# Kernel tuning notes

Measured on AMD Instinct MI355X. Metric: run time of the kernel, lower is better.

Reference implementation:

```python
import jax, jax.numpy as jnp
import numpy as np

NUM_ENTITIES = 100000
NUM_RELATIONS = 8
HIDDEN = 128
N_NODES = 100000
N_EDGES = 500000


def setup_inputs() -> dict:
    key = jax.random.key(0)
    ks = jax.random.split(key, 10)
    scale = 1.0 / np.sqrt(HIDDEN)
    inp = {
        "x_ids": jax.random.randint(ks[0], (N_NODES,), 0, NUM_ENTITIES),
        "edge_index": jax.random.randint(ks[1], (2, N_EDGES), 0, N_NODES),
        "edge_type": jax.random.randint(ks[2], (N_EDGES,), 0, NUM_RELATIONS),
        "emb": jax.random.normal(ks[3], (NUM_ENTITIES, HIDDEN), jnp.float32),
        "W1": jax.random.normal(ks[4], (NUM_RELATIONS, HIDDEN, HIDDEN), jnp.float32) * scale,
        "root1": jax.random.normal(ks[5], (HIDDEN, HIDDEN), jnp.float32) * scale,
        "b1": jnp.zeros((HIDDEN,), jnp.float32),
        "W2": jax.random.normal(ks[6], (NUM_RELATIONS, HIDDEN, HIDDEN), jnp.float32) * scale,
        "root2": jax.random.normal(ks[7], (HIDDEN, HIDDEN), jnp.float32) * scale,
        "b2": jnp.zeros((HIDDEN,), jnp.float32),
    }
    return inp


def rgcn_conv(x, edge_index, edge_type, W, root, bias):
    # x: [N, d]; W: [R, d, d]; PyG RGCNConv with aggr='mean' (per-relation mean)
    N, d = x.shape
    R = W.shape[0]
    src, dst = edge_index[0], edge_index[1]
    # transform every node under every relation: [N, R, d]
    h = jnp.einsum('nd,rdf->nrf', x, W)
    msg = h[src, edge_type]                       # [E, d] gather per edge
    seg = dst * R + edge_type                     # composite (node, relation) segment id
    sums = jax.ops.segment_sum(msg, seg, num_segments=N * R)
    cnt = jax.ops.segment_sum(jnp.ones((msg.shape[0], 1), x.dtype), seg, num_segments=N * R)
    agg = (sums / jnp.maximum(cnt, 1.0)).reshape(N, R, d).sum(axis=1)
    return agg + x @ root + bias


def reference(x_ids, edge_index, edge_type, emb, W1, root1, b1, W2, root2, b2):
    x = emb[x_ids]                                # embedding lookup [N, d]
    x = rgcn_conv(x, edge_index, edge_type, W1, root1, b1)
    x = jax.nn.relu(x)
    x = rgcn_conv(x, edge_index, edge_type, W2, root2, b2)
    return jax.nn.sigmoid(x)
```

## Files before the change

### kernel.cpp

```cpp
#include <hip/hip_runtime.h>

#define HD 128
#define RNUM 8
#define SCAN_BS 2048

typedef __attribute__((ext_vector_type(8))) short short8;
typedef __attribute__((ext_vector_type(4))) float float4e;

__device__ __forceinline__ unsigned short f2bf(float f) {
    unsigned int u = __float_as_uint(f);
    u += 0x7fffu + ((u >> 16) & 1u);
    return (unsigned short)(u >> 16);
}

__device__ __forceinline__ void acc2(float4e& a, unsigned int u, int i) {
    a[i]     += __uint_as_float(u << 16);
    a[i + 1] += __uint_as_float(u & 0xffff0000u);
}

__device__ __forceinline__ void gload_lds16(const void* g, void* l) {
    __builtin_amdgcn_global_load_lds(
        (const __attribute__((address_space(1))) void*)g,
        (__attribute__((address_space(3))) void*)l, 16, 0, 0);
}

__global__ void zero_i(int* __restrict__ p, int n) {
    int g = blockIdx.x * blockDim.x + threadIdx.x;
    if (g < n) p[g] = 0;
}

__global__ void tobf16_kernel(const float* __restrict__ in, unsigned short* __restrict__ out,
                              long long n8) {
    long long g = (long long)blockIdx.x * blockDim.x + threadIdx.x;
    if (g >= n8) return;
    const float4* p = (const float4*)(in + g * 8);
    float4 v0 = p[0], v1 = p[1];
    uint4 o;
    o.x = (unsigned int)f2bf(v0.x) | ((unsigned int)f2bf(v0.y) << 16);
    o.y = (unsigned int)f2bf(v0.z) | ((unsigned int)f2bf(v0.w) << 16);
    o.z = (unsigned int)f2bf(v1.x) | ((unsigned int)f2bf(v1.y) << 16);
    o.w = (unsigned int)f2bf(v1.z) | ((unsigned int)f2bf(v1.w) << 16);
    *(uint4*)(out + g * 8) = o;
}

__global__ void count_kernel(const int* __restrict__ ei, const int* __restrict__ et,
                             int* __restrict__ cnt, int E, int N) {
    int e = blockIdx.x * blockDim.x + threadIdx.x;
    if (e < E) atomicAdd(&cnt[et[e] * N + ei[E + e]], 1);
}

__global__ void scan1(const int* __restrict__ in, int* __restrict__ out,
                      int* __restrict__ bsum, int n) {
    __shared__ int s[256];
    const int tid = threadIdx.x;
    const int base = blockIdx.x * SCAN_BS + tid * 8;
    int v[8];
    int sum = 0;
#pragma unroll
    for (int j = 0; j < 8; j++) {
        int x = (base + j < n) ? in[base + j] : 0;
        v[j] = sum;
        sum += x;
    }
    s[tid] = sum;
    __syncthreads();
    for (int off = 1; off < 256; off <<= 1) {
        int tv = (tid >= off) ? s[tid - off] : 0;
        __syncthreads();
        if (tid >= off) s[tid] += tv;
        __syncthreads();
    }
    int excl = (tid > 0) ? s[tid - 1] : 0;
    if (tid == 255) bsum[blockIdx.x] = s[255];
#pragma unroll
    for (int j = 0; j < 8; j++)
        if (base + j < n) out[base + j] = v[j] + excl;
}

__global__ void scan2(int* __restrict__ bsum, int nb) {
    __shared__ int s[512];
    const int tid = threadIdx.x;
    s[tid] = (tid < nb) ? bsum[tid] : 0;
    __syncthreads();
    for (int off = 1; off < 512; off <<= 1) {
        int tv = (tid >= off) ? s[tid - off] : 0;
        __syncthreads();
        if (tid >= off) s[tid] += tv;
        __syncthreads();
    }
    if (tid < nb) bsum[tid] = (tid > 0) ? s[tid - 1] : 0;
}

__global__ void scan3(int* __restrict__ out, int* __restrict__ cur,
                      const int* __restrict__ bsum, int n) {
    const int base = blockIdx.x * SCAN_BS + threadIdx.x * 8;
    const int add = bsum[blockIdx.x];
#pragma unroll
    for (int j = 0; j < 8; j++) {
        int i = base + j;
        if (i < n) {
            int v = out[i] + add;
            out[i] = v;
            cur[i] = v;
        }
    }
}

__global__ void fill_kernel(const int* __restrict__ ei, const int* __restrict__ et,
                            const int* __restrict__ ids,
                            int* __restrict__ cur, int* __restrict__ col,
                            int* __restrict__ colE, int E, int N) {
    int e = blockIdx.x * blockDim.x + threadIdx.x;
    if (e < E) {
        int src = ei[e];
        int pos = atomicAdd(&cur[et[e] * N + ei[E + e]], 1);
        col[pos] = src;
        colE[pos] = ids[src];
    }
}

__global__ void wt_all(const float* __restrict__ W1, const float* __restrict__ r1,
                       const float* __restrict__ W2, const float* __restrict__ r2,
                       unsigned short* __restrict__ WT) {
    int g = blockIdx.x * blockDim.x + threadIdx.x;
    if (g >= 18 * 16384) return;
    int mat = g >> 14;
    int idx = g & 16383;
    int d = idx >> 7;
    int f = idx & 127;
    const float* src;
    int m;
    if (mat < 8)       { src = W1; m = mat; }
    else if (mat == 8) { src = r1; m = 0; }
    else if (mat < 17) { src = W2; m = mat - 9; }
    else               { src = r2; m = 0; }
    WT[mat * 16384 + f * 128 + d] = f2bf(src[(size_t)m * 16384 + d * 128 + f]);
}

template <bool HAS_IDX, int ACT>
__launch_bounds__(256, 3)
__global__ void rgcn_fused(const int* __restrict__ row_start, const int* __restrict__ col,
                           const int* __restrict__ ids,
                           const unsigned short* __restrict__ x16,
                           const unsigned short* __restrict__ WT,
                           const float* __restrict__ bias,
                           void* __restrict__ CoutV, int N, int E) {
    __shared__ unsigned short As[64 * 128];
    __shared__ unsigned short Ws[128 * 128];

    const int tid = threadIdx.x;
    const int block0 = blockIdx.x * 64;
    const int w = tid >> 6;
    const int lane = tid & 63;
    const int ln15 = lane & 15;
    const int quad = lane >> 4;
    const int rowbase = (w & 1) * 32;
    const int colbase = (w >> 1) * 64;
    const int grp = tid >> 3;
    const int sub8 = tid & 7;

    float4e acc[2][4];
#pragma unroll
    for (int i = 0; i < 2; i++)
#pragma unroll
        for (int j = 0; j < 4; j++)
#pragma unroll
            for (int q = 0; q < 4; q++) acc[i][j][q] = 0.0f;

    for (int s = 0; s < 9; s++) {
        {
            const unsigned short* Wsrc = WT + s * 16384;
#pragma unroll
            for (int i = 0; i < 8; i++) {
                int c = i * 256 + tid;
                int f = c >> 4;
                int cc = c & 15;
                const void* src = (const void*)(Wsrc + f * 128 + ((cc ^ (f & 15)) << 3));
                int cbase = i * 256 + (tid & ~63);
                gload_lds16(src, (char*)Ws + (size_t)cbase * 16);
            }
        }
        if (s < RNUM) {
#pragma unroll 1
            for (int half = 0; half < 2; half++) {
                const int row = grp + half * 32;
                const int dst = block0 + row;
                float4e a0 = {0.f, 0.f, 0.f, 0.f};
                float4e a1 = {0.f, 0.f, 0.f, 0.f};
                float4e a2 = {0.f, 0.f, 0.f, 0.f};
                float4e a3 = {0.f, 0.f, 0.f, 0.f};
                float inv = 0.f;
                if (dst < N) {
                    int seg = s * N + dst;
                    int s0 = row_start[seg];
                    int s1 = (seg == RNUM * N - 1) ? E : row_start[seg + 1];
                    if (s1 > s0) inv = 1.0f / (float)(s1 - s0);
                    for (int e = s0; e < s1; e++) {
                        int c = col[e];
                        const uint4* xp = (const uint4*)(x16 + (size_t)c * HD + sub8 * 16);
                        uint4 v0 = xp[0];
                        uint4 v1 = xp[1];
                        acc2(a0, v0.x, 0); acc2(a0, v0.y, 2);
                        acc2(a1, v0.z, 0); acc2(a1, v0.w, 2);
                        acc2(a2, v1.x, 0); acc2(a2, v1.y, 2);
                        acc2(a3, v1.z, 0); acc2(a3, v1.w, 2);
                    }
                }
                a0 *= inv; a1 *= inv; a2 *= inv; a3 *= inv;
                uint4 o0, o1;
                o0.x = (unsigned int)f2bf(a0[0]) | ((unsigned int)f2bf(a0[1]) << 16);
                o0.y = (unsigned int)f2bf(a0[2]) | ((unsigned int)f2bf(a0[3]) << 16);
                o0.z = (unsigned int)f2bf(a1[0]) | ((unsigned int)f2bf(a1[1]) << 16);
                o0.w = (unsigned int)f2bf(a1[2]) | ((unsigned int)f2bf(a1[3]) << 16);
                o1.x = (unsigned int)f2bf(a2[0]) | ((unsigned int)f2bf(a2[1]) << 16);
                o1.y = (unsigned int)f2bf(a2[2]) | ((unsigned int)f2bf(a2[3]) << 16);
                o1.z = (unsigned int)f2bf(a3[0]) | ((unsigned int)f2bf(a3[1]) << 16);
                o1.w = (unsigned int)f2bf(a3[2]) | ((unsigned int)f2bf(a3[3]) << 16);
                const int ck0 = sub8 * 2;
                *(uint4*)&As[row * 128 + ((ck0 ^ (row & 15)) << 3)] = o0;
                *(uint4*)&As[row * 128 + (((ck0 + 1) ^ (row & 15)) << 3)] = o1;
            }
        } else {
#pragma unroll 1
            for (int half = 0; half < 2; half++) {
                const int row = grp + half * 32;
                const int dst = block0 + row;
                uint4 o0 = {0u, 0u, 0u, 0u}, o1 = {0u, 0u, 0u, 0u};
                if (dst < N) {
                    int srcn = HAS_IDX ? ids[dst] : dst;
                    const uint4* xp = (const uint4*)(x16 + (size_t)srcn * HD + sub8 * 16);
                    o0 = xp[0];
                    o1 = xp[1];
                }
                const int ck0 = sub8 * 2;
                *(uint4*)&As[row * 128 + ((ck0 ^ (row & 15)) << 3)] = o0;
                *(uint4*)&As[row * 128 + (((ck0 + 1) ^ (row & 15)) << 3)] = o1;
            }
        }
        __syncthreads();

#pragma unroll
        for (int k0 = 0; k0 < 4; k0++) {
            short8 af[2], bf[4];
            const int ck = k0 * 4 + quad;
#pragma unroll
            for (int rt = 0; rt < 2; rt++) {
                int m = rowbase + rt * 16 + ln15;
                af[rt] = *(const short8*)&As[m * 128 + ((ck ^ (m & 15)) << 3)];
            }
#pragma unroll
            for (int ct = 0; ct < 4; ct++) {
                int n = colbase + ct * 16 + ln15;
                bf[ct] = *(const short8*)&Ws[n * 128 + ((ck ^ (n & 15)) << 3)];
            }
#pragma unroll
            for (int rt = 0; rt < 2; rt++)
#pragma unroll
                for (int ct = 0; ct < 4; ct++)
                    acc[rt][ct] = __builtin_amdgcn_mfma_f32_16x16x32_bf16(
                        af[rt], bf[ct], acc[rt][ct], 0, 0, 0);
        }
        __syncthreads();
    }

#pragma unroll
    for (int ct = 0; ct < 4; ct++) {
        int ncol = colbase + ct * 16 + ln15;
        float bv = bias[ncol];
#pragma unroll
        for (int rt = 0; rt < 2; rt++) {
#pragma unroll
            for (int rg = 0; rg < 4; rg++) {
                int rowg = block0 + rowbase + rt * 16 + quad * 4 + rg;
                if (rowg < N) {
                    float v = acc[rt][ct][rg] + bv;
                    if (ACT == 0) {
                        v = fmaxf(v, 0.0f);
                        ((unsigned short*)CoutV)[(size_t)rowg * HD + ncol] = f2bf(v);
                    } else {
                        v = 1.0f / (1.0f + expf(-v));
                        ((float*)CoutV)[(size_t)rowg * HD + ncol] = v;
                    }
                }
            }
        }
    }
}

extern "C" void kernel_launch(void* const* d_in, const int* in_sizes, int n_in,
                              void* d_out, int out_size, void* d_ws, size_t ws_size,
                              hipStream_t stream) {
    const int*   x_ids = (const int*)d_in[0];
    const int*   ei    = (const int*)d_in[1];
    const int*   et    = (const int*)d_in[2];
    const float* emb   = (const float*)d_in[3];
    const float* W1    = (const float*)d_in[4];
    const float* root1 = (const float*)d_in[5];
    const float* b1    = (const float*)d_in[6];
    const float* W2    = (const float*)d_in[7];
    const float* root2 = (const float*)d_in[8];
    const float* b2    = (const float*)d_in[9];

    const int N = in_sizes[0];
    const int E = in_sizes[1] / 2;
    const int NS = RNUM * N;
    const long long embElems = (long long)in_sizes[3];
    float* out = (float*)d_out;

    char* ws = (char*)d_ws;
    size_t off = 0;
    int* row_start = (int*)(ws + off); off += (size_t)NS * 4;
    int* col       = (int*)(ws + off); off += (size_t)E * 4;
    int* colE      = (int*)(ws + off); off += (size_t)E * 4;
    int* bsum      = (int*)(ws + off); off += 4096;
    unsigned short* WT    = (unsigned short*)(ws + off); off += (size_t)18 * 16384 * 2;
    unsigned short* emb16 = (unsigned short*)(ws + off); off += (size_t)embElems * 2;
    unsigned short* z16   = (unsigned short*)(ws + off); off += (size_t)N * HD * 2;
    int* cur = (int*)z16;

    const int scanBlocks = (NS + SCAN_BS - 1) / SCAN_BS;
    const int layerGrid = (N + 63) / 64;

    zero_i<<<(NS + 255) / 256, 256, 0, stream>>>(cur, NS);
    count_kernel<<<(E + 255) / 256, 256, 0, stream>>>(ei, et, cur, E, N);
    scan1<<<scanBlocks, 256, 0, stream>>>(cur, row_start, bsum, NS);
    scan2<<<1, 512, 0, stream>>>(bsum, scanBlocks);
    scan3<<<scanBlocks, 256, 0, stream>>>(row_start, cur, bsum, NS);
    fill_kernel<<<(E + 255) / 256, 256, 0, stream>>>(ei, et, x_ids, cur, col, colE, E, N);

    wt_all<<<(18 * 16384 + 255) / 256, 256, 0, stream>>>(W1, root1, W2, root2, WT);

    {
        long long n8 = embElems / 8;
        tobf16_kernel<<<(unsigned int)((n8 + 255) / 256), 256, 0, stream>>>(emb, emb16, n8);
    }

    rgcn_fused<true, 0><<<layerGrid, 256, 0, stream>>>(
        row_start, colE, x_ids, emb16, WT, b1, (void*)z16, N, E);
    rgcn_fused<false, 1><<<layerGrid, 256, 0, stream>>>(
        row_start, col, nullptr, z16, WT + 9 * 16384, b2, (void*)out, N, E);
}
```

Measured before the change: 459.9 us.

## Use node-major CSR segments, 4-thread row gather, and merge prep kernels

Segment ids become dst*8+rel instead of rel*N+dst, so each node's eight relation ranges sit next to each other in row_start and the end offset is read directly from a sentinel entry. The fused layer kernel now assigns four threads per destination row, each loading 64 bytes of a neighbour's features, which replaces the two-pass half loop. The root-weight stage is moved out of the relation loop. The weight transpose and embedding bf16 conversion are merged into one launch to save a kernel launch. Fewer threads per row means fewer gathers in flight per row and more register pressure from eight accumulators.

Result: faster. 407.8 us (-11.3%).

```diff
diff --git a/kernel.cpp b/kernel.cpp
--- a/kernel.cpp
+++ b/kernel.cpp
@@ -13,6 +13,10 @@
     return (unsigned short)(u >> 16);
 }
 
+__device__ __forceinline__ unsigned int pk2(float lo, float hi) {
+    return (unsigned int)f2bf(lo) | ((unsigned int)f2bf(hi) << 16);
+}
+
 __device__ __forceinline__ void acc2(float4e& a, unsigned int u, int i) {
     a[i]     += __uint_as_float(u << 16);
     a[i + 1] += __uint_as_float(u & 0xffff0000u);
@@ -29,24 +33,43 @@
     if (g < n) p[g] = 0;
 }
 
-__global__ void tobf16_kernel(const float* __restrict__ in, unsigned short* __restrict__ out,
-                              long long n8) {
+__global__ void prep_kernel(const float* __restrict__ W1, const float* __restrict__ r1,
+                            const float* __restrict__ W2, const float* __restrict__ r2,
+                            unsigned short* __restrict__ WT,
+                            const float* __restrict__ emb, unsigned short* __restrict__ emb16,
+                            long long n8) {
     long long g = (long long)blockIdx.x * blockDim.x + threadIdx.x;
-    if (g >= n8) return;
-    const float4* p = (const float4*)(in + g * 8);
-    float4 v0 = p[0], v1 = p[1];
-    uint4 o;
-    o.x = (unsigned int)f2bf(v0.x) | ((unsigned int)f2bf(v0.y) << 16);
-    o.y = (unsigned int)f2bf(v0.z) | ((unsigned int)f2bf(v0.w) << 16);
-    o.z = (unsigned int)f2bf(v1.x) | ((unsigned int)f2bf(v1.y) << 16);
-    o.w = (unsigned int)f2bf(v1.z) | ((unsigned int)f2bf(v1.w) << 16);
-    *(uint4*)(out + g * 8) = o;
+    if (g < 18 * 16384) {
+        int gi = (int)g;
+        int mat = gi >> 14;
+        int idx = gi & 16383;
+        int d = idx >> 7;
+        int f = idx & 127;
+        const float* src;
+        int m;
+        if (mat < 8)       { src = W1; m = mat; }
+        else if (mat == 8) { src = r1; m = 0; }
+        else if (mat < 17) { src = W2; m = mat - 9; }
+        else               { src = r2; m = 0; }
+        WT[mat * 16384 + f * 128 + d] = f2bf(src[(size_t)m * 16384 + d * 128 + f]);
+    }
+    long long h = g - 18 * 16384;
+    if (h >= 0 && h < n8) {
+        const float4* p = (const float4*)(emb + h * 8);
+        float4 v0 = p[0], v1 = p[1];
+        uint4 o;
+        o.x = pk2(v0.x, v0.y);
+        o.y = pk2(v0.z, v0.w);
+        o.z = pk2(v1.x, v1.y);
+        o.w = pk2(v1.z, v1.w);
+        *(uint4*)(emb16 + h * 8) = o;
+    }
 }
 
 __global__ void count_kernel(const int* __restrict__ ei, const int* __restrict__ et,
                              int* __restrict__ cnt, int E, int N) {
     int e = blockIdx.x * blockDim.x + threadIdx.x;
-    if (e < E) atomicAdd(&cnt[et[e] * N + ei[E + e]], 1);
+    if (e < E) atomicAdd(&cnt[ei[E + e] * RNUM + et[e]], 1);
 }
 
 __global__ void scan1(const int* __restrict__ in, int* __restrict__ out,
@@ -109,32 +132,16 @@
 __global__ void fill_kernel(const int* __restrict__ ei, const int* __restrict__ et,
                             const int* __restrict__ ids,
                             int* __restrict__ cur, int* __restrict__ col,
-                            int* __restrict__ colE, int E, int N) {
+                            int* __restrict__ colE, int* __restrict__ row_start,
+                            int E, int N) {
     int e = blockIdx.x * blockDim.x + threadIdx.x;
+    if (e == 0) row_start[RNUM * N] = E;
     if (e < E) {
         int src = ei[e];
-        int pos = atomicAdd(&cur[et[e] * N + ei[E + e]], 1);
+        int pos = atomicAdd(&cur[ei[E + e] * RNUM + et[e]], 1);
         col[pos] = src;
         colE[pos] = ids[src];
     }
-}
-
-__global__ void wt_all(const float* __restrict__ W1, const float* __restrict__ r1,
-                       const float* __restrict__ W2, const float* __restrict__ r2,
-                       unsigned short* __restrict__ WT) {
-    int g = blockIdx.x * blockDim.x + threadIdx.x;
-    if (g >= 18 * 16384) return;
-    int mat = g >> 14;
-    int idx = g & 16383;
-    int d = idx >> 7;
-    int f = idx & 127;
-    const float* src;
-    int m;
-    if (mat < 8)       { src = W1; m = mat; }
-    else if (mat == 8) { src = r1; m = 0; }
-    else if (mat < 17) { src = W2; m = mat - 9; }
-    else               { src = r2; m = 0; }
-    WT[mat * 16384 + f * 128 + d] = f2bf(src[(size_t)m * 16384 + d * 128 + f]);
 }
 
 template <bool HAS_IDX, int ACT>
@@ -156,8 +163,10 @@
     const int quad = lane >> 4;
     const int rowbase = (w & 1) * 32;
     const int colbase = (w >> 1) * 64;
-    const int grp = tid >> 3;
-    const int sub8 = tid & 7;
+    const int grp = tid >> 2;
+    const int sub4 = tid & 3;
+    const int mydst = block0 + grp;
+    const bool rowok = (mydst < N);
 
     float4e acc[2][4];
 #pragma unroll
@@ -167,7 +176,8 @@
 #pragma unroll
             for (int q = 0; q < 4; q++) acc[i][j][q] = 0.0f;
 
-    for (int s = 0; s < 9; s++) {
+#pragma unroll 1
+    for (int s = 0; s < RNUM; s++) {
         {
             const unsigned short* Wsrc = WT + s * 16384;
 #pragma unroll
@@ -180,65 +190,91 @@
                 gload_lds16(src, (char*)Ws + (size_t)cbase * 16);
             }
         }
-        if (s < RNUM) {
-#pragma unroll 1
-            for (int half = 0; half < 2; half++) {
-                const int row = grp + half * 32;
-                const int dst = block0 + row;
-                float4e a0 = {0.f, 0.f, 0.f, 0.f};
-                float4e a1 = {0.f, 0.f, 0.f, 0.f};
-                float4e a2 = {0.f, 0.f, 0.f, 0.f};
-                float4e a3 = {0.f, 0.f, 0.f, 0.f};
-                float inv = 0.f;
-                if (dst < N) {
-                    int seg = s * N + dst;
-                    int s0 = row_start[seg];
-                    int s1 = (seg == RNUM * N - 1) ? E : row_start[seg + 1];
-                    if (s1 > s0) inv = 1.0f / (float)(s1 - s0);
-                    for (int e = s0; e < s1; e++) {
-                        int c = col[e];
-                        const uint4* xp = (const uint4*)(x16 + (size_t)c * HD + sub8 * 16);
-                        uint4 v0 = xp[0];
-                        uint4 v1 = xp[1];
-                        acc2(a0, v0.x, 0); acc2(a0, v0.y, 2);
-                        acc2(a1, v0.z, 0); acc2(a1, v0.w, 2);
-                        acc2(a2, v1.x, 0); acc2(a2, v1.y, 2);
-                        acc2(a3, v1.z, 0); acc2(a3, v1.w, 2);
-                    }
-                }
-                a0 *= inv; a1 *= inv; a2 *= inv; a3 *= inv;
-                uint4 o0, o1;
-                o0.x = (unsigned int)f2bf(a0[0]) | ((unsigned int)f2bf(a0[1]) << 16);
-                o0.y = (unsigned int)f2bf(a0[2]) | ((unsigned int)f2bf(a0[3]) << 16);
-                o0.z = (unsigned int)f2bf(a1[0]) | ((unsigned int)f2bf(a1[1]) << 16);
-                o0.w = (unsigned int)f2bf(a1[2]) | ((unsigned int)f2bf(a1[3]) << 16);
-                o1.x = (unsigned int)f2bf(a2[0]) | ((unsigned int)f2bf(a2[1]) << 16);
-                o1.y = (unsigned int)f2bf(a2[2]) | ((unsigned int)f2bf(a2[3]) << 16);
-                o1.z = (unsigned int)f2bf(a3[0]) | ((unsigned int)f2bf(a3[1]) << 16);
-                o1.w = (unsigned int)f2bf(a3[2]) | ((unsigned int)f2bf(a3[3]) << 16);
-                const int ck0 = sub8 * 2;
-                *(uint4*)&As[row * 128 + ((ck0 ^ (row & 15)) << 3)] = o0;
-                *(uint4*)&As[row * 128 + (((ck0 + 1) ^ (row & 15)) << 3)] = o1;
-            }
-        } else {
-#pragma unroll 1
-            for (int half = 0; half < 2; half++) {
-                const int row = grp + half * 32;
-                const int dst = block0 + row;
-                uint4 o0 = {0u, 0u, 0u, 0u}, o1 = {0u, 0u, 0u, 0u};
-                if (dst < N) {
-                    int srcn = HAS_IDX ? ids[dst] : dst;
-                    const uint4* xp = (const uint4*)(x16 + (size_t)srcn * HD + sub8 * 16);
-                    o0 = xp[0];
-                    o1 = xp[1];
-                }
-                const int ck0 = sub8 * 2;
-                *(uint4*)&As[row * 128 + ((ck0 ^ (row & 15)) << 3)] = o0;
-                *(uint4*)&As[row * 128 + (((ck0 + 1) ^ (row & 15)) << 3)] = o1;
-            }
-        }
-        __syncthreads();
-
+        {
+            float4e a[8];
+#pragma unroll
+            for (int j = 0; j < 8; j++) a[j] = (float4e){0.f, 0.f, 0.f, 0.f};
+            int s0 = 0, s1 = 0;
+            if (rowok) {
+                s0 = row_start[mydst * 8 + s];
+                s1 = row_start[mydst * 8 + s + 1];
+            }
+            const float inv = (s1 > s0) ? 1.0f / (float)(s1 - s0) : 0.0f;
+            for (int e = s0; e < s1; e++) {
+                int c = col[e];
+                const uint4* xp = (const uint4*)(x16 + (size_t)c * HD + sub4 * 32);
+                uint4 v0 = xp[0], v1 = xp[1], v2 = xp[2], v3 = xp[3];
+                acc2(a[0], v0.x, 0); acc2(a[0], v0.y, 2);
+                acc2(a[1], v0.z, 0); acc2(a[1], v0.w, 2);
+                acc2(a[2], v1.x, 0); acc2(a[2], v1.y, 2);
+                acc2(a[3], v1.z, 0); acc2(a[3], v1.w, 2);
+                acc2(a[4], v2.x, 0); acc2(a[4], v2.y, 2);
+                acc2(a[5], v2.z, 0); acc2(a[5], v2.w, 2);
+                acc2(a[6], v3.x, 0); acc2(a[6], v3.y, 2);
+                acc2(a[7], v3.z, 0); acc2(a[7], v3.w, 2);
+            }
+#pragma unroll
+            for (int j = 0; j < 8; j++) a[j] *= inv;
+#pragma unroll
+            for (int j = 0; j < 4; j++) {
+                uint4 o;
+                o.x = pk2(a[2 * j][0], a[2 * j][1]);
+                o.y = pk2(a[2 * j][2], a[2 * j][3]);
+                o.z = pk2(a[2 * j + 1][0], a[2 * j + 1][1]);
+                o.w = pk2(a[2 * j + 1][2], a[2 * j + 1][3]);
+                int ck = sub4 * 4 + j;
+                *(uint4*)&As[grp * 128 + ((ck ^ (grp & 15)) << 3)] = o;
+            }
+        }
+        __syncthreads();
+
+#pragma unroll
+        for (int k0 = 0; k0 < 4; k0++) {
+            short8 af[2], bf[4];
+            const int ck = k0 * 4 + quad;
+#pragma unroll
+            for (int rt = 0; rt < 2; rt++) {
+                int m = rowbase + rt * 16 + ln15;
+                af[rt] = *(const short8*)&As[m * 128 + ((ck ^ (m & 15)) << 3)];
+            }
+#pragma unroll
+            for (int ct = 0; ct < 4; ct++) {
+                int n = colbase + ct * 16 + ln15;
+                bf[ct] = *(const short8*)&Ws[n * 128 + ((ck ^ (n & 15)) << 3)];
+            }
+#pragma unroll
+            for (int rt = 0; rt < 2; rt++)
+#pragma unroll
+                for (int ct = 0; ct < 4; ct++)
+                    acc[rt][ct] = __builtin_amdgcn_mfma_f32_16x16x32_bf16(
+                        af[rt], bf[ct], acc[rt][ct], 0, 0, 0);
+        }
+        __syncthreads();
+    }
+
+    {
+        const unsigned short* Wsrc = WT + RNUM * 16384;
+#pragma unroll
+        for (int i = 0; i < 8; i++) {
+            int c = i * 256 + tid;
+            int f = c >> 4;
+            int cc = c & 15;
+            const void* src = (const void*)(Wsrc + f * 128 + ((cc ^ (f & 15)) << 3));
+            int cbase = i * 256 + (tid & ~63);
+            gload_lds16(src, (char*)Ws + (size_t)cbase * 16);
+        }
+        uint4 o0 = {0u, 0u, 0u, 0u}, o1 = o0, o2 = o0, o3 = o0;
+        if (rowok) {
+            int srcn = HAS_IDX ? ids[mydst] : mydst;
+            const uint4* xp = (const uint4*)(x16 + (size_t)srcn * HD + sub4 * 32);
+            o0 = xp[0]; o1 = xp[1]; o2 = xp[2]; o3 = xp[3];
+        }
+        const int ck0 = sub4 * 4;
+        *(uint4*)&As[grp * 128 + (((ck0 + 0) ^ (grp & 15)) << 3)] = o0;
+        *(uint4*)&As[grp * 128 + (((ck0 + 1) ^ (grp & 15)) << 3)] = o1;
+        *(uint4*)&As[grp * 128 + (((ck0 + 2) ^ (grp & 15)) << 3)] = o2;
+        *(uint4*)&As[grp * 128 + (((ck0 + 3) ^ (grp & 15)) << 3)] = o3;
+        __syncthreads();
 #pragma unroll
         for (int k0 = 0; k0 < 4; k0++) {
             short8 af[2], bf[4];
@@ -309,7 +345,7 @@
 
     char* ws = (char*)d_ws;
     size_t off = 0;
-    int* row_start = (int*)(ws + off); off += (size_t)NS * 4;
+    int* row_start = (int*)(ws + off); off += (size_t)(NS + 4) * 4;
     int* col       = (int*)(ws + off); off += (size_t)E * 4;
     int* colE      = (int*)(ws + off); off += (size_t)E * 4;
     int* bsum      = (int*)(ws + off); off += 4096;
@@ -326,13 +362,14 @@
     scan1<<<scanBlocks, 256, 0, stream>>>(cur, row_start, bsum, NS);
     scan2<<<1, 512, 0, stream>>>(bsum, scanBlocks);
     scan3<<<scanBlocks, 256, 0, stream>>>(row_start, cur, bsum, NS);
-    fill_kernel<<<(E + 255) / 256, 256, 0, stream>>>(ei, et, x_ids, cur, col, colE, E, N);
-
-    wt_all<<<(18 * 16384 + 255) / 256, 256, 0, stream>>>(W1, root1, W2, root2, WT);
+    fill_kernel<<<(E + 255) / 256, 256, 0, stream>>>(ei, et, x_ids, cur, col, colE,
+                                                     row_start, E, N);
 
     {
         long long n8 = embElems / 8;
-        tobf16_kernel<<<(unsigned int)((n8 + 255) / 256), 256, 0, stream>>>(emb, emb16, n8);
+        long long total = 18 * 16384 + n8;
+        prep_kernel<<<(unsigned int)((total + 255) / 256), 256, 0, stream>>>(
+            W1, root1, W2, root2, WT, emb, emb16, n8);
     }
 
     rgcn_fused<true, 0><<<layerGrid, 256, 0, stream>>>(
```
